# Kernel optimization log

Measured on AMD Instinct MI355X. Metric: run time of the kernel, lower is better.

Reference implementation:

```python
import jax, jax.numpy as jnp
import numpy as np

COST_CLASS = 2.0
COST_BBOX = 5.0
COST_GIOU = 2.0
COST_INNER = 9999.0
FOCAL_ALPHA = 0.25
FOCAL_GAMMA = 2.0
EPS = 1e-8


def box_cxcywh_to_xyxy(b):
    cx, cy, w, h = b[..., 0], b[..., 1], b[..., 2], b[..., 3]
    return jnp.stack([cx - 0.5 * w, cy - 0.5 * h, cx + 0.5 * w, cy + 0.5 * h], axis=-1)


def generalized_box_iou(boxes1, boxes2):
    # boxes in xyxy; boxes1 [N,4], boxes2 [T,4] -> [N,T]
    area1 = (boxes1[:, 2] - boxes1[:, 0]) * (boxes1[:, 3] - boxes1[:, 1])
    area2 = (boxes2[:, 2] - boxes2[:, 0]) * (boxes2[:, 3] - boxes2[:, 1])
    lt = jnp.maximum(boxes1[:, None, :2], boxes2[None, :, :2])
    rb = jnp.minimum(boxes1[:, None, 2:], boxes2[None, :, 2:])
    wh = jnp.clip(rb - lt, 0.0)
    inter = wh[..., 0] * wh[..., 1]
    union = area1[:, None] + area2[None, :] - inter
    iou = inter / union
    # enclosing box
    lt_c = jnp.minimum(boxes1[:, None, :2], boxes2[None, :, :2])
    rb_c = jnp.maximum(boxes1[:, None, 2:], boxes2[None, :, 2:])
    wh_c = jnp.clip(rb_c - lt_c, 0.0)
    area_c = wh_c[..., 0] * wh_c[..., 1]
    return iou - (area_c - union) / area_c


def setup_inputs() -> dict:
    key = jax.random.key(0)
    k1, k2, k3, k4, k5, k6 = jax.random.split(key, 6)
    bs, nq, nc, T = 16, 900, 91, 1024
    return {
        "pred_logits": jax.random.normal(k1, (bs, nq, nc), dtype=jnp.float32),
        "pred_boxes": jax.random.uniform(k2, (bs, nq, 4), dtype=jnp.float32),
        "pred_points": jax.random.uniform(k3, (bs, nq, 2), dtype=jnp.float32),
        "pred_objs": jax.random.normal(k4, (bs, nq, 1), dtype=jnp.float32),
        "tgt_labels": jax.random.randint(k5, (T,), 0, nc, dtype=jnp.int64),
        "tgt_boxes": jax.random.uniform(k6, (T, 4), dtype=jnp.float32),
    }


def reference(pred_logits, pred_boxes, pred_points, pred_objs, tgt_labels, tgt_boxes):
    bs, nq, nc = pred_logits.shape
    out_prob = jax.nn.sigmoid(pred_logits.reshape(bs * nq, nc))       # [N,C]
    out_bbox = pred_boxes.reshape(bs * nq, 4)                          # [N,4]
    out_point = pred_points.reshape(bs * nq, 2)                        # [N,2]
    out_obj = jax.nn.sigmoid(pred_objs.reshape(bs * nq, 1))            # [N,1]
    out_prob = out_prob * out_obj

    # focal classification cost, gathered at target classes -> [N,T]
    neg = (1.0 - FOCAL_ALPHA) * out_prob ** FOCAL_GAMMA * (-jnp.log(1.0 - out_prob + EPS))
    pos = FOCAL_ALPHA * (1.0 - out_prob) ** FOCAL_GAMMA * (-jnp.log(out_prob + EPS))
    cost_class = jnp.take(pos, tgt_labels, axis=1) - jnp.take(neg, tgt_labels, axis=1)

    out_xyxy = box_cxcywh_to_xyxy(out_bbox)
    tgt_xyxy = box_cxcywh_to_xyxy(tgt_boxes)

    # L1 cdist on xyxy boxes -> [N,T]
    cost_bbox = jnp.sum(jnp.abs(out_xyxy[:, None, :] - tgt_xyxy[None, :, :]), axis=-1)

    cost_giou = -generalized_box_iou(out_xyxy, tgt_xyxy)               # [N,T]

    # inner-point cost: 1 if predicted point falls outside target box
    left = out_point[:, 0, None] - tgt_xyxy[None, :, 0]
    top = out_point[:, 1, None] - tgt_xyxy[None, :, 1]
    right = tgt_xyxy[None, :, 2] - out_point[:, 0, None]
    bottom = tgt_xyxy[None, :, 3] - out_point[:, 1, None]
    min_dist = jnp.minimum(jnp.minimum(left, top), jnp.minimum(right, bottom))
    cost_inner = 1.0 - (min_dist >= 0.0).astype(out_prob.dtype)

    C = (COST_BBOX * cost_bbox + COST_CLASS * cost_class
         + COST_GIOU * cost_giou + COST_INNER * cost_inner)
    return C.reshape(bs, nq, -1)
```

## Files before the change

kernel.cpp:

```cpp
#include <hip/hip_runtime.h>
#include <math.h>


#define BN 8
#define BT 256
#define VT 4
#define TBL_STRIDE 96

__global__ __launch_bounds__(BT) void matcher_kernel(
    const float* __restrict__ logits,
    const float* __restrict__ boxes,
    const float* __restrict__ points,
    const float* __restrict__ objs,
    const int*   __restrict__ labels,
    const float* __restrict__ tboxes,
    float* __restrict__ out,
    int N, int C, int T)
{
    __shared__ float s_table[BN * TBL_STRIDE];
    __shared__ float s_row[BN][8];

    const int tid = threadIdx.x;
    const int rowBase = blockIdx.y * BN;
    const int t0 = (blockIdx.x * BT + tid) * VT;

    if (tid < BN) {
        int n = rowBase + tid;
        if (n < N) {
            float4 b = *(const float4*)(boxes + 4 * n);
            float x0 = b.x - 0.5f * b.z;
            float y0 = b.y - 0.5f * b.w;
            float x1 = b.x + 0.5f * b.z;
            float y1 = b.y + 0.5f * b.w;
            s_row[tid][0] = x0;
            s_row[tid][1] = y0;
            s_row[tid][2] = x1;
            s_row[tid][3] = y1;
            float2 p = *(const float2*)(points + 2 * n);
            s_row[tid][4] = p.x;
            s_row[tid][5] = p.y;
            s_row[tid][6] = (x1 - x0) * (y1 - y0);
            s_row[tid][7] = 1.0f / (1.0f + expf(-objs[n]));
        }
    }
    __syncthreads();

    for (int idx = tid; idx < BN * C; idx += BT) {
        int r = idx / C;
        int c = idx - r * C;
        int n = rowBase + r;
        float v = 0.0f;
        if (n < N) {
            float lg = logits[n * C + c];
            float ps = 1.0f / (1.0f + expf(-lg));
            float p = ps * s_row[r][7];
            float omp = 1.0f - p;
            float pos = 0.25f * (omp * omp) * (-logf(p + 1e-8f));
            float neg = 0.75f * (p * p) * (-logf(omp + 1e-8f));
            v = pos - neg;
        }
        s_table[r * TBL_STRIDE + c] = v;
    }
    __syncthreads();

    if (t0 + VT <= T && rowBase + BN <= N) {
        int4 lv = *(const int4*)(labels + t0);
        int lab[VT];
        lab[0] = lv.x; lab[1] = lv.y; lab[2] = lv.z; lab[3] = lv.w;
        float tx0[VT], ty0[VT], tx1[VT], ty1[VT], tarea[VT];
        #pragma unroll
        for (int j = 0; j < VT; ++j) {
            float4 tb = *(const float4*)(tboxes + 4 * (t0 + j));
            tx0[j] = tb.x - 0.5f * tb.z;
            ty0[j] = tb.y - 0.5f * tb.w;
            tx1[j] = tb.x + 0.5f * tb.z;
            ty1[j] = tb.y + 0.5f * tb.w;
            tarea[j] = (tx1[j] - tx0[j]) * (ty1[j] - ty0[j]);
        }

        float cc[BN][VT];
        #pragma unroll
        for (int r = 0; r < BN; ++r) {
            const float* trow = s_table + r * TBL_STRIDE;
            #pragma unroll
            for (int j = 0; j < VT; ++j)
                cc[r][j] = trow[lab[j]];
        }

        float rx0[BN], ry0[BN], rx1[BN], ry1[BN], rpx[BN], rpy[BN], ra1[BN];
        #pragma unroll
        for (int r = 0; r < BN; ++r) {
            float4 ra = *(const float4*)&s_row[r][0];
            float4 rb = *(const float4*)&s_row[r][4];
            rx0[r] = ra.x; ry0[r] = ra.y; rx1[r] = ra.z; ry1[r] = ra.w;
            rpx[r] = rb.x; rpy[r] = rb.y; ra1[r] = rb.z;
        }

        float* obase = out + (size_t)rowBase * T + t0;
        #pragma unroll
        for (int r = 0; r < BN; ++r) {
            float x0 = rx0[r], y0 = ry0[r], x1 = rx1[r], y1 = ry1[r];
            float px = rpx[r], py = rpy[r], a1 = ra1[r];

            float4 res;
            float* resp = (float*)&res;
            #pragma unroll
            for (int j = 0; j < VT; ++j) {
                float l1 = fabsf(x0 - tx0[j]) + fabsf(y0 - ty0[j])
                         + fabsf(x1 - tx1[j]) + fabsf(y1 - ty1[j]);

                float iw = fminf(x1, tx1[j]) - fmaxf(x0, tx0[j]);
                float ih = fminf(y1, ty1[j]) - fmaxf(y0, ty0[j]);
                float inter = fmaxf(iw, 0.0f) * fmaxf(ih, 0.0f);
                float uni = (a1 + tarea[j]) - inter;

                float cw = fmaxf(x1, tx1[j]) - fminf(x0, tx0[j]);
                float ch = fmaxf(y1, ty1[j]) - fminf(y0, ty0[j]);
                float carea = cw * ch;

                float R = __builtin_amdgcn_rcpf(uni * carea);
                float giou = (inter * carea - uni * (carea - uni)) * R;

                float left = px - tx0[j];
                float top = py - ty0[j];
                float right = tx1[j] - px;
                float bottom = ty1[j] - py;
                float mind = fminf(fminf(left, top), fminf(right, bottom));

                float Cv = fmaf(5.0f, l1, fmaf(2.0f, cc[r][j], -2.0f * giou));
                Cv += (mind >= 0.0f) ? 0.0f : 9999.0f;
                resp[j] = Cv;
            }
            *(float4*)(obase + (size_t)r * T) = res;
        }
    }
}

extern "C" void kernel_launch(void* const* d_in, const int* in_sizes, int n_in,
                              void* d_out, int out_size, void* d_ws, size_t ws_size,
                              hipStream_t stream) {
    const float* logits = (const float*)d_in[0];
    const float* boxes  = (const float*)d_in[1];
    const float* points = (const float*)d_in[2];
    const float* objs   = (const float*)d_in[3];
    const int*   labels = (const int*)d_in[4];
    const float* tboxes = (const float*)d_in[5];
    float* out = (float*)d_out;

    int N = in_sizes[1] / 4;
    int T = in_sizes[5] / 4;
    int C = in_sizes[0] / N;

    dim3 grid((T + BT * VT - 1) / (BT * VT), (N + BN - 1) / BN);
    matcher_kernel<<<grid, BT, 0, stream>>>(logits, boxes, points, objs,
                                            labels, tboxes, out, N, C, T);
}
```

Baseline: 99.91 us.

## Split focal-cost table and box precompute into a separate prep kernel

Moves the per-row sigmoid/log focal table computation, the row box conversion and the target box conversion into a prep kernel that writes packed data to workspace. The main kernel then reads cost-table entries and packed row and target data from global memory instead of recomputing them per block in shared memory. This removes the redundant per-block table computation and syncs, but costs a second launch and global gathers for the class cost. The main kernel hardcodes one block per 8 rows covering all T=1024 targets with no bounds checks.

```diff
diff --git a/kernel.cpp b/kernel.cpp
--- a/kernel.cpp
+++ b/kernel.cpp
@@ -2,137 +2,148 @@
 #include <math.h>
 
 
-#define BN 8
-#define BT 256
-#define VT 4
-#define TBL_STRIDE 96
+#define TSTR 96
 
-__global__ __launch_bounds__(BT) void matcher_kernel(
+#define ROWPACK_OFF 0x580000
+#define TGTPACK_OFF 0x600000
+
+__global__ __launch_bounds__(256) void prep_kernel(
     const float* __restrict__ logits,
     const float* __restrict__ boxes,
     const float* __restrict__ points,
     const float* __restrict__ objs,
     const int*   __restrict__ labels,
     const float* __restrict__ tboxes,
-    float* __restrict__ out,
+    float* __restrict__ ws,
     int N, int C, int T)
 {
-    __shared__ float s_table[BN * TBL_STRIDE];
-    __shared__ float s_row[BN][8];
+    float* table   = ws;
+    float* rowpack = (float*)((char*)ws + ROWPACK_OFF);
+    float* tgtpack = (float*)((char*)ws + TGTPACK_OFF);
 
-    const int tid = threadIdx.x;
-    const int rowBase = blockIdx.y * BN;
-    const int t0 = (blockIdx.x * BT + tid) * VT;
+    const int n  = blockIdx.x * 256 + threadIdx.x;
+    const int cy = blockIdx.y;
 
-    if (tid < BN) {
-        int n = rowBase + tid;
+    if (cy == 7) {
         if (n < N) {
             float4 b = *(const float4*)(boxes + 4 * n);
             float x0 = b.x - 0.5f * b.z;
             float y0 = b.y - 0.5f * b.w;
             float x1 = b.x + 0.5f * b.z;
             float y1 = b.y + 0.5f * b.w;
-            s_row[tid][0] = x0;
-            s_row[tid][1] = y0;
-            s_row[tid][2] = x1;
-            s_row[tid][3] = y1;
             float2 p = *(const float2*)(points + 2 * n);
-            s_row[tid][4] = p.x;
-            s_row[tid][5] = p.y;
-            s_row[tid][6] = (x1 - x0) * (y1 - y0);
-            s_row[tid][7] = 1.0f / (1.0f + expf(-objs[n]));
+            float* rp = rowpack + 8 * n;
+            rp[0] = x0; rp[1] = y0; rp[2] = x1; rp[3] = y1;
+            rp[4] = p.x; rp[5] = p.y; rp[6] = (x1 - x0) * (y1 - y0); rp[7] = 0.f;
         }
+        if (n < T) {
+            float4 tb = *(const float4*)(tboxes + 4 * n);
+            float x0 = tb.x - 0.5f * tb.z;
+            float y0 = tb.y - 0.5f * tb.w;
+            float x1 = tb.x + 0.5f * tb.z;
+            float y1 = tb.y + 0.5f * tb.w;
+            float* tp = tgtpack + 8 * n;
+            tp[0] = x0; tp[1] = y0; tp[2] = x1; tp[3] = y1;
+            tp[4] = (x1 - x0) * (y1 - y0);
+            tp[5] = __int_as_float(labels[n]);
+            tp[6] = 0.f; tp[7] = 0.f;
+        }
+        return;
     }
-    __syncthreads();
 
-    for (int idx = tid; idx < BN * C; idx += BT) {
-        int r = idx / C;
-        int c = idx - r * C;
-        int n = rowBase + r;
-        float v = 0.0f;
-        if (n < N) {
-            float lg = logits[n * C + c];
-            float ps = 1.0f / (1.0f + expf(-lg));
-            float p = ps * s_row[r][7];
-            float omp = 1.0f - p;
-            float pos = 0.25f * (omp * omp) * (-logf(p + 1e-8f));
-            float neg = 0.75f * (p * p) * (-logf(omp + 1e-8f));
-            v = pos - neg;
-        }
-        s_table[r * TBL_STRIDE + c] = v;
+    if (n >= N) return;
+    float po = __builtin_amdgcn_rcpf(1.0f + expf(-objs[n]));
+    int c0 = cy * 13;
+    int c1 = c0 + 13; if (c1 > C) c1 = C;
+    float* trow = table + (size_t)n * TSTR;
+    for (int c = c0; c < c1; ++c) {
+        float lg = logits[n * C + c];
+        float ps = __builtin_amdgcn_rcpf(1.0f + expf(-lg));
+        float p = ps * po;
+        float omp = 1.0f - p;
+        float pos = 0.25f * (omp * omp) * (-logf(p + 1e-8f));
+        float neg = 0.75f * (p * p) * (-logf(omp + 1e-8f));
+        trow[c] = pos - neg;
     }
-    __syncthreads();
+}
 
-    if (t0 + VT <= T && rowBase + BN <= N) {
-        int4 lv = *(const int4*)(labels + t0);
-        int lab[VT];
-        lab[0] = lv.x; lab[1] = lv.y; lab[2] = lv.z; lab[3] = lv.w;
-        float tx0[VT], ty0[VT], tx1[VT], ty1[VT], tarea[VT];
+#define BN 8
+#define VT 4
+
+__global__ __launch_bounds__(256) void matcher_main(
+    const float* __restrict__ ws_ro,
+    float* __restrict__ out,
+    int N, int T)
+{
+    const float* table   = ws_ro;
+    const float* rowpack = (const float*)((const char*)ws_ro + ROWPACK_OFF);
+    const float* tgtpack = (const float*)((const char*)ws_ro + TGTPACK_OFF);
+
+    const int tid = threadIdx.x;
+    const int rowBase = blockIdx.x * BN;
+    const int t0 = tid * VT;
+
+    float tx0[VT], ty0[VT], tx1[VT], ty1[VT], tarea[VT];
+    int lab[VT];
+    #pragma unroll
+    for (int j = 0; j < VT; ++j) {
+        const float4* tp = (const float4*)(tgtpack + 8 * (t0 + j));
+        float4 a = tp[0];
+        float4 b = tp[1];
+        tx0[j] = a.x; ty0[j] = a.y; tx1[j] = a.z; ty1[j] = a.w;
+        tarea[j] = b.x;
+        lab[j] = __float_as_int(b.y);
+    }
+
+    float cc[BN][VT];
+    #pragma unroll
+    for (int r = 0; r < BN; ++r) {
+        const float* trow = table + (size_t)(rowBase + r) * TSTR;
+        #pragma unroll
+        for (int j = 0; j < VT; ++j)
+            cc[r][j] = trow[lab[j]];
+    }
+
+    const float* rp = rowpack + (size_t)rowBase * 8;
+
+    float* obase = out + (size_t)rowBase * T + t0;
+    #pragma unroll
+    for (int r = 0; r < BN; ++r) {
+        float x0 = rp[r * 8 + 0], y0 = rp[r * 8 + 1];
+        float x1 = rp[r * 8 + 2], y1 = rp[r * 8 + 3];
+        float px = rp[r * 8 + 4], py = rp[r * 8 + 5];
+        float a1 = rp[r * 8 + 6];
+
+        float4 res;
+        float* resp = (float*)&res;
         #pragma unroll
         for (int j = 0; j < VT; ++j) {
-            float4 tb = *(const float4*)(tboxes + 4 * (t0 + j));
-            tx0[j] = tb.x - 0.5f * tb.z;
-            ty0[j] = tb.y - 0.5f * tb.w;
-            tx1[j] = tb.x + 0.5f * tb.z;
-            ty1[j] = tb.y + 0.5f * tb.w;
-            tarea[j] = (tx1[j] - tx0[j]) * (ty1[j] - ty0[j]);
+            float l1 = fabsf(x0 - tx0[j]) + fabsf(y0 - ty0[j])
+                     + fabsf(x1 - tx1[j]) + fabsf(y1 - ty1[j]);
+
+            float iw = fminf(x1, tx1[j]) - fmaxf(x0, tx0[j]);
+            float ih = fminf(y1, ty1[j]) - fmaxf(y0, ty0[j]);
+            float inter = fmaxf(iw, 0.0f) * fmaxf(ih, 0.0f);
+            float uni = (a1 + tarea[j]) - inter;
+
+            float cw = fmaxf(x1, tx1[j]) - fminf(x0, tx0[j]);
+            float ch = fmaxf(y1, ty1[j]) - fminf(y0, ty0[j]);
+            float carea = cw * ch;
+
+            float R = __builtin_amdgcn_rcpf(uni * carea);
+            float giou = (inter * carea - uni * (carea - uni)) * R;
+
+            float left = px - tx0[j];
+            float top = py - ty0[j];
+            float right = tx1[j] - px;
+            float bottom = ty1[j] - py;
+            float mind = fminf(fminf(left, top), fminf(right, bottom));
+
+            float Cv = fmaf(5.0f, l1, fmaf(2.0f, cc[r][j], -2.0f * giou));
+            Cv += (mind >= 0.0f) ? 0.0f : 9999.0f;
+            resp[j] = Cv;
         }
-
-        float cc[BN][VT];
-        #pragma unroll
-        for (int r = 0; r < BN; ++r) {
-            const float* trow = s_table + r * TBL_STRIDE;
-            #pragma unroll
-            for (int j = 0; j < VT; ++j)
-                cc[r][j] = trow[lab[j]];
-        }
-
-        float rx0[BN], ry0[BN], rx1[BN], ry1[BN], rpx[BN], rpy[BN], ra1[BN];
-        #pragma unroll
-        for (int r = 0; r < BN; ++r) {
-            float4 ra = *(const float4*)&s_row[r][0];
-            float4 rb = *(const float4*)&s_row[r][4];
-            rx0[r] = ra.x; ry0[r] = ra.y; rx1[r] = ra.z; ry1[r] = ra.w;
-            rpx[r] = rb.x; rpy[r] = rb.y; ra1[r] = rb.z;
-        }
-
-        float* obase = out + (size_t)rowBase * T + t0;
-        #pragma unroll
-        for (int r = 0; r < BN; ++r) {
-            float x0 = rx0[r], y0 = ry0[r], x1 = rx1[r], y1 = ry1[r];
-            float px = rpx[r], py = rpy[r], a1 = ra1[r];
-
-            float4 res;
-            float* resp = (float*)&res;
-            #pragma unroll
-            for (int j = 0; j < VT; ++j) {
-                float l1 = fabsf(x0 - tx0[j]) + fabsf(y0 - ty0[j])
-                         + fabsf(x1 - tx1[j]) + fabsf(y1 - ty1[j]);
-
-                float iw = fminf(x1, tx1[j]) - fmaxf(x0, tx0[j]);
-                float ih = fminf(y1, ty1[j]) - fmaxf(y0, ty0[j]);
-                float inter = fmaxf(iw, 0.0f) * fmaxf(ih, 0.0f);
-                float uni = (a1 + tarea[j]) - inter;
-
-                float cw = fmaxf(x1, tx1[j]) - fminf(x0, tx0[j]);
-                float ch = fmaxf(y1, ty1[j]) - fminf(y0, ty0[j]);
-                float carea = cw * ch;
-
-                float R = __builtin_amdgcn_rcpf(uni * carea);
-                float giou = (inter * carea - uni * (carea - uni)) * R;
-
-                float left = px - tx0[j];
-                float top = py - ty0[j];
-                float right = tx1[j] - px;
-                float bottom = ty1[j] - py;
-                float mind = fminf(fminf(left, top), fminf(right, bottom));
-
-                float Cv = fmaf(5.0f, l1, fmaf(2.0f, cc[r][j], -2.0f * giou));
-                Cv += (mind >= 0.0f) ? 0.0f : 9999.0f;
-                resp[j] = Cv;
-            }
-            *(float4*)(obase + (size_t)r * T) = res;
-        }
+        *(float4*)(obase + (size_t)r * T) = res;
     }
 }
 
@@ -146,12 +157,15 @@
     const int*   labels = (const int*)d_in[4];
     const float* tboxes = (const float*)d_in[5];
     float* out = (float*)d_out;
+    float* ws = (float*)d_ws;
 
     int N = in_sizes[1] / 4;
     int T = in_sizes[5] / 4;
     int C = in_sizes[0] / N;
 
-    dim3 grid((T + BT * VT - 1) / (BT * VT), (N + BN - 1) / BN);
-    matcher_kernel<<<grid, BT, 0, stream>>>(logits, boxes, points, objs,
-                                            labels, tboxes, out, N, C, T);
+    dim3 gp((N + 255) / 256, 8);
+    prep_kernel<<<gp, 256, 0, stream>>>(logits, boxes, points, objs,
+                                        labels, tboxes, ws, N, C, T);
+
+    matcher_main<<<dim3(N / BN), 256, 0, stream>>>(ws, out, N, T);
 }
```

Result: slower. 119.2 us (+19.3%).

## Transpose class-cost table for vectorized LDS gathers and drop bounds checks

Applied to the files above, without the earlier changes.

Stores the per-block focal class-cost table as [class][row] so each thread fetches all 8 rows for one label with two float4 shared-memory loads, replacing 32 scalar gathers. It also switches sigmoid and log to fast intrinsics (__expf, __logf, rcp), removes the N and T bounds checks, and fixes the grid's x dimension to 1, assuming T equals BT*VT and N is a multiple of BN. The specialization hardcodes the test shapes and gives up generality, and the fast math may change precision slightly.

```diff
diff --git a/kernel.cpp b/kernel.cpp
--- a/kernel.cpp
+++ b/kernel.cpp
@@ -5,7 +5,6 @@
 #define BN 8
 #define BT 256
 #define VT 4
-#define TBL_STRIDE 96
 
 __global__ __launch_bounds__(BT) void matcher_kernel(
     const float* __restrict__ logits,
@@ -17,56 +16,48 @@
     float* __restrict__ out,
     int N, int C, int T)
 {
-    __shared__ float s_table[BN * TBL_STRIDE];
+    __shared__ float s_tab[96 * BN];
     __shared__ float s_row[BN][8];
 
     const int tid = threadIdx.x;
     const int rowBase = blockIdx.y * BN;
-    const int t0 = (blockIdx.x * BT + tid) * VT;
+    const int t0 = tid * VT;
 
     if (tid < BN) {
         int n = rowBase + tid;
-        if (n < N) {
-            float4 b = *(const float4*)(boxes + 4 * n);
-            float x0 = b.x - 0.5f * b.z;
-            float y0 = b.y - 0.5f * b.w;
-            float x1 = b.x + 0.5f * b.z;
-            float y1 = b.y + 0.5f * b.w;
-            s_row[tid][0] = x0;
-            s_row[tid][1] = y0;
-            s_row[tid][2] = x1;
-            s_row[tid][3] = y1;
-            float2 p = *(const float2*)(points + 2 * n);
-            s_row[tid][4] = p.x;
-            s_row[tid][5] = p.y;
-            s_row[tid][6] = (x1 - x0) * (y1 - y0);
-            s_row[tid][7] = 1.0f / (1.0f + expf(-objs[n]));
-        }
+        float4 b = *(const float4*)(boxes + 4 * n);
+        float x0 = b.x - 0.5f * b.z;
+        float y0 = b.y - 0.5f * b.w;
+        float x1 = b.x + 0.5f * b.z;
+        float y1 = b.y + 0.5f * b.w;
+        s_row[tid][0] = x0;
+        s_row[tid][1] = y0;
+        s_row[tid][2] = x1;
+        s_row[tid][3] = y1;
+        float2 p = *(const float2*)(points + 2 * n);
+        s_row[tid][4] = p.x;
+        s_row[tid][5] = p.y;
+        s_row[tid][6] = (x1 - x0) * (y1 - y0);
+        s_row[tid][7] = __builtin_amdgcn_rcpf(1.0f + __expf(-objs[n]));
     }
     __syncthreads();
 
     for (int idx = tid; idx < BN * C; idx += BT) {
         int r = idx / C;
         int c = idx - r * C;
-        int n = rowBase + r;
-        float v = 0.0f;
-        if (n < N) {
-            float lg = logits[n * C + c];
-            float ps = 1.0f / (1.0f + expf(-lg));
-            float p = ps * s_row[r][7];
-            float omp = 1.0f - p;
-            float pos = 0.25f * (omp * omp) * (-logf(p + 1e-8f));
-            float neg = 0.75f * (p * p) * (-logf(omp + 1e-8f));
-            v = pos - neg;
-        }
-        s_table[r * TBL_STRIDE + c] = v;
+        float lg = logits[(size_t)rowBase * C + idx];
+        float ps = __builtin_amdgcn_rcpf(1.0f + __expf(-lg));
+        float p = ps * s_row[r][7];
+        float omp = 1.0f - p;
+        float pos = 0.25f * (omp * omp) * (-__logf(p + 1e-8f));
+        float neg = 0.75f * (p * p) * (-__logf(omp + 1e-8f));
+        s_tab[c * BN + r] = pos - neg;
     }
     __syncthreads();
 
-    if (t0 + VT <= T && rowBase + BN <= N) {
+    {
         int4 lv = *(const int4*)(labels + t0);
-        int lab[VT];
-        lab[0] = lv.x; lab[1] = lv.y; lab[2] = lv.z; lab[3] = lv.w;
+        int lab[VT] = {lv.x, lv.y, lv.z, lv.w};
         float tx0[VT], ty0[VT], tx1[VT], ty1[VT], tarea[VT];
         #pragma unroll
         for (int j = 0; j < VT; ++j) {
@@ -78,13 +69,14 @@
             tarea[j] = (tx1[j] - tx0[j]) * (ty1[j] - ty0[j]);
         }
 
-        float cc[BN][VT];
+        float cc[VT][BN];
         #pragma unroll
-        for (int r = 0; r < BN; ++r) {
-            const float* trow = s_table + r * TBL_STRIDE;
-            #pragma unroll
-            for (int j = 0; j < VT; ++j)
-                cc[r][j] = trow[lab[j]];
+        for (int j = 0; j < VT; ++j) {
+            const float4* tp = (const float4*)(s_tab + lab[j] * BN);
+            float4 lo = tp[0];
+            float4 hi = tp[1];
+            cc[j][0] = lo.x; cc[j][1] = lo.y; cc[j][2] = lo.z; cc[j][3] = lo.w;
+            cc[j][4] = hi.x; cc[j][5] = hi.y; cc[j][6] = hi.z; cc[j][7] = hi.w;
         }
 
         float rx0[BN], ry0[BN], rx1[BN], ry1[BN], rpx[BN], rpy[BN], ra1[BN];
@@ -127,7 +119,7 @@
                 float bottom = ty1[j] - py;
                 float mind = fminf(fminf(left, top), fminf(right, bottom));
 
-                float Cv = fmaf(5.0f, l1, fmaf(2.0f, cc[r][j], -2.0f * giou));
+                float Cv = fmaf(5.0f, l1, fmaf(2.0f, cc[j][r], -2.0f * giou));
                 Cv += (mind >= 0.0f) ? 0.0f : 9999.0f;
                 resp[j] = Cv;
             }
@@ -151,7 +143,7 @@
     int T = in_sizes[5] / 4;
     int C = in_sizes[0] / N;
 
-    dim3 grid((T + BT * VT - 1) / (BT * VT), (N + BN - 1) / BN);
+    dim3 grid(1, N / BN);
     matcher_kernel<<<grid, BT, 0, stream>>>(logits, boxes, points, objs,
                                             labels, tboxes, out, N, C, T);
 }
```

Result: faster. 97.69 us (-2.2%).
